# Optimization experiments

Measured on AMD Instinct MI355X. Metric: run time of the kernel, lower is better.

## Reference

```python
import jax, jax.numpy as jnp
import numpy as np

S_STA = 32          # s_sta_dim
N_TS = 4            # n_timesteps
NUM_FREQ = 4        # NeRF PE octaves -> 2 + 2*2*4 = 18 PE channels
EPS_NORM = 1e-12    # torch F.normalize default eps


def pos_enc_concat(v):
    # v: (B, C, H, W) -> concat NeRF positional encoding of pixel grid on channel dim
    B, C, H, W = v.shape
    ys = jnp.linspace(-1.0, 1.0, H)
    xs = jnp.linspace(-1.0, 1.0, W)
    coords = jnp.stack(jnp.meshgrid(ys, xs, indexing='ij'), axis=0)  # (2, H, W)
    feats = [coords]
    for i in range(NUM_FREQ):
        f = (2.0 ** i) * jnp.pi * coords
        feats.append(jnp.sin(f))
        feats.append(jnp.cos(f))
    pe = jnp.concatenate(feats, axis=0).astype(v.dtype)              # (18, H, W)
    pe = jnp.broadcast_to(pe[None], (B,) + pe.shape)
    return jnp.concatenate([v, pe], axis=1)


def setup_inputs() -> dict:
    key = jax.random.key(0)
    k1, k2, k3 = jax.random.split(key, 3)
    ch = 128
    x = jax.random.normal(k1, (4, 4, 12, ch, 24, 24), dtype=jnp.float32)
    Wv = jax.random.normal(k2, (ch, ch), dtype=jnp.float32) / np.float32(np.sqrt(ch))
    bv = jax.random.normal(k3, (ch,), dtype=jnp.float32) * 0.01
    return {"x": x, "Wv": Wv, "bv": bv, "temp": 1}


def reference(x, Wv, bv, temp):
    bs, N, T, ch, h, w = x.shape
    BN, hw = bs * N, h * w
    scale = ch ** (-0.5)
    xf = x.reshape(BN, T, ch, h, w)

    # F.normalize(p=2, dim=-3): L2-normalize over channel dim
    nrm = jnp.sqrt(jnp.sum(xf * xf, axis=2, keepdims=True))
    x_att = xf / jnp.maximum(nrm, EPS_NORM)

    qs = x_att[:, 1:].reshape(BN * (T - 1), ch, hw)
    ks = x_att[:, :-1].reshape(BN * (T - 1), ch, hw)
    energy = jnp.einsum('bcn,bcm->bnm', qs, ks).reshape(BN, T - 1, hw, hw) * scale
    attn = jax.nn.softmax(energy / temp, axis=-1)       # (BN, T-1, hw, hw)

    # to_v: 1x1 conv then NeRF PE concat
    v = jnp.einsum('oc,btchw->btohw', Wv, xf) + bv[None, None, :, None, None]
    v = pos_enc_concat(v.reshape(BN * T, ch, h, w))     # (BN*T, ch+18, h, w)
    vs_pe = v.reshape(BN, T, -1, hw)                    # (BN, T, C_v, hw)

    Tp = T - N_TS + 1
    acc = vs_pe[:, :Tp, S_STA:]                         # (BN, Tp, C_v-S_STA, hw)
    for t in range(N_TS - 1):                           # small fixed recurrence depth
        cs = vs_pe[:, t + 1:t + 1 + Tp, S_STA:]
        ca = attn[:, t:t + Tp]
        prop = jnp.einsum('btcm,btnm->btcn', acc, ca)
        acc = jnp.concatenate([cs, prop], axis=2)
    return acc
```

## Files before the change

kernel.cpp:

```cpp
#include <hip/hip_runtime.h>
#include <math.h>

#define BN 16
#define T 12
#define CH 128
#define HW 576
#define TM1 11
#define TP 9
#define CCS 114

typedef __attribute__((ext_vector_type(8))) short bf16x8;
typedef __attribute__((ext_vector_type(4))) float floatx4;

__device__ inline float b2f(unsigned short u) {
    unsigned int v = ((unsigned int)u) << 16;
    return __builtin_bit_cast(float, v);
}
__device__ inline unsigned short f2b(float f) {
    unsigned int v = __builtin_bit_cast(unsigned int, f);
    unsigned int r = (v + 0x7FFFu + ((v >> 16) & 1u)) >> 16;
    return (unsigned short)r;
}

__device__ __forceinline__ void async_copy16(void* lds, const void* g) {
    __builtin_amdgcn_global_load_lds(
        (const __attribute__((address_space(1))) unsigned int*)g,
        (__attribute__((address_space(3))) unsigned int*)lds,
        16, 0, 0);
}

__global__ __launch_bounds__(256) void k_norm_t(const float* __restrict__ x,
                                                unsigned short* __restrict__ xT) {
    int bt = blockIdx.x / 9;
    int p0 = (blockIdx.x % 9) * 64;
    int t = threadIdx.x;
    int lane = t & 63, wave = t >> 6;
    int pq = t & 15;
    int cg = t >> 4;
    const float* src = x + (size_t)bt * CH * HW + (size_t)(cg * 8) * HW + p0 + pq * 4;

    floatx4 v[8];
    float s0 = 0.f, s1 = 0.f, s2 = 0.f, s3 = 0.f;
#pragma unroll
    for (int j = 0; j < 8; j++) {
        v[j] = *(const floatx4*)(src + (size_t)j * HW);
        s0 = fmaf(v[j][0], v[j][0], s0);
        s1 = fmaf(v[j][1], v[j][1], s1);
        s2 = fmaf(v[j][2], v[j][2], s2);
        s3 = fmaf(v[j][3], v[j][3], s3);
    }
#pragma unroll
    for (int m = 16; m < 64; m <<= 1) {
        s0 += __shfl_xor(s0, m);
        s1 += __shfl_xor(s1, m);
        s2 += __shfl_xor(s2, m);
        s3 += __shfl_xor(s3, m);
    }
    __shared__ float smP[4][16][4];
    __shared__ float smI[64];
    if (lane < 16) {
        smP[wave][lane][0] = s0; smP[wave][lane][1] = s1;
        smP[wave][lane][2] = s2; smP[wave][lane][3] = s3;
    }
    __syncthreads();
    if (t < 64) {
        int q = t >> 2, k = t & 3;
        float tot = smP[0][q][k] + smP[1][q][k] + smP[2][q][k] + smP[3][q][k];
        smI[t] = 1.0f / fmaxf(sqrtf(tot), 1e-12f);
    }
    __syncthreads();
    unsigned short* dst = xT + ((size_t)bt * HW + p0 + pq * 4) * CH + cg * 8;
#pragma unroll
    for (int k = 0; k < 4; k++) {
        float inv = smI[pq * 4 + k];
        union { unsigned short u[8]; uint4 q4; } pk;
#pragma unroll
        for (int j = 0; j < 8; j++) pk.u[j] = f2b(v[j][k] * inv);
        *(uint4*)(dst + (size_t)k * CH) = pk.q4;
    }
}

__global__ __launch_bounds__(256, 2) void k_energysm(const unsigned short* __restrict__ xT,
                                                     unsigned short* __restrict__ attn,
                                                     const int* __restrict__ temp) {
    int nwg = gridDim.x;
    int wg = (blockIdx.x & 7) * (nwg >> 3) + (blockIdx.x >> 3);
    int z = wg / 18, nt = wg % 18;
    int b = z / TM1, ti = z % TM1;
    const unsigned short* Q = xT + (size_t)(b * T + ti + 1) * HW * CH;
    const unsigned short* K = xT + (size_t)(b * T + ti) * HW * CH;
    unsigned short* A = attn + (size_t)z * HW * HW;
    int n0 = nt * 32;

    int lane = threadIdx.x & 63, wave = threadIdx.x >> 6;
    int fr = lane & 15, hi = lane >> 4;
    int koff = hi * 8;
    int m0 = wave * 144;

    bf16x8 af[4][2];
#pragma unroll
    for (int k0 = 0; k0 < 4; k0++)
#pragma unroll
        for (int fi = 0; fi < 2; fi++)
            af[k0][fi] = *(const bf16x8*)(Q + (size_t)(n0 + fi * 16 + fr) * CH + k0 * 32 + koff);

    floatx4 acc[2][9] = {};
#pragma unroll
    for (int k0 = 0; k0 < 4; k0++) {
        bf16x8 bfr[9];
#pragma unroll
        for (int j = 0; j < 9; j++)
            bfr[j] = *(const bf16x8*)(K + (size_t)(m0 + j * 16 + fr) * CH + k0 * 32 + koff);
#pragma unroll
        for (int fi = 0; fi < 2; fi++)
#pragma unroll
            for (int j = 0; j < 9; j++)
                acc[fi][j] = __builtin_amdgcn_mfma_f32_16x16x32_bf16(af[k0][fi], bfr[j], acc[fi][j], 0, 0, 0);
    }

    __shared__ float smMax[4][32];
    __shared__ float smSum[4][32];
    float sc = 0.08838834764831845f / (float)temp[0];

    float pm[2][4];
#pragma unroll
    for (int fi = 0; fi < 2; fi++)
#pragma unroll
        for (int reg = 0; reg < 4; reg++) {
            float m = acc[fi][0][reg];
#pragma unroll
            for (int j = 1; j < 9; j++) m = fmaxf(m, acc[fi][j][reg]);
#pragma unroll
            for (int msk = 1; msk < 16; msk <<= 1) m = fmaxf(m, __shfl_xor(m, msk));
            pm[fi][reg] = m;
        }
    if (fr == 0) {
#pragma unroll
        for (int fi = 0; fi < 2; fi++)
#pragma unroll
            for (int reg = 0; reg < 4; reg++)
                smMax[wave][fi * 16 + hi * 4 + reg] = pm[fi][reg];
    }
    __syncthreads();

    float rmax[2][4];
#pragma unroll
    for (int fi = 0; fi < 2; fi++)
#pragma unroll
        for (int reg = 0; reg < 4; reg++) {
            int row = fi * 16 + hi * 4 + reg;
            rmax[fi][reg] = fmaxf(fmaxf(smMax[0][row], smMax[1][row]),
                                  fmaxf(smMax[2][row], smMax[3][row]));
        }

    float ps[2][4];
#pragma unroll
    for (int fi = 0; fi < 2; fi++)
#pragma unroll
        for (int reg = 0; reg < 4; reg++) {
            float s = 0.f;
#pragma unroll
            for (int j = 0; j < 9; j++) {
                float e = __expf(sc * (acc[fi][j][reg] - rmax[fi][reg]));
                acc[fi][j][reg] = e;
                s += e;
            }
#pragma unroll
            for (int msk = 1; msk < 16; msk <<= 1) s += __shfl_xor(s, msk);
            ps[fi][reg] = s;
        }
    if (fr == 0) {
#pragma unroll
        for (int fi = 0; fi < 2; fi++)
#pragma unroll
            for (int reg = 0; reg < 4; reg++)
                smSum[wave][fi * 16 + hi * 4 + reg] = ps[fi][reg];
    }
    __syncthreads();

#pragma unroll
    for (int fi = 0; fi < 2; fi++)
#pragma unroll
        for (int reg = 0; reg < 4; reg++) {
            int row = fi * 16 + hi * 4 + reg;
            float inv = 1.0f / (smSum[0][row] + smSum[1][row] + smSum[2][row] + smSum[3][row]);
            int n = n0 + row;
#pragma unroll
            for (int j = 0; j < 9; j++)
                A[(size_t)n * HW + m0 + j * 16 + fr] = f2b(acc[fi][j][reg] * inv);
        }
}

__global__ __launch_bounds__(256) void k_vgemm(const float* __restrict__ x,
                                               const float* __restrict__ Wv,
                                               const float* __restrict__ bv,
                                               unsigned short* __restrict__ cs16,
                                               float* __restrict__ out) {
    int bt = blockIdx.z;
    int b = bt / T, t = bt % T;
    const float* X = x + (size_t)bt * CH * HW;
    unsigned short* C16 = cs16 + (size_t)bt * CCS * HW;
    float* O = (t >= 3) ? out + (size_t)(b * TP + t - 3) * 456 * HW : nullptr;
    int m0 = blockIdx.y * 64, n0 = blockIdx.x * 64;
    __shared__ float As[16][66];
    __shared__ float Bs[16][66];
    int tid = threadIdx.x;
    int kq = tid % 16, lr = tid / 16;
    int tx = tid % 16, ty = tid / 16;
    int lp = tid % 64, lc = tid / 64;
    float acc[4][4] = {};
    for (int c0 = 0; c0 < CH; c0 += 16) {
#pragma unroll
        for (int i = 0; i < 4; i++) {
            int r = m0 + lr + 16 * i;
            As[kq][lr + 16 * i] = (r < 96) ? Wv[(size_t)(32 + r) * CH + c0 + kq] : 0.f;
        }
#pragma unroll
        for (int i = 0; i < 4; i++) {
            int c = lc + 4 * i;
            Bs[c][lp] = X[(size_t)(c0 + c) * HW + n0 + lp];
        }
        __syncthreads();
#pragma unroll
        for (int kk = 0; kk < 16; kk++) {
            float2 a01 = *(const float2*)&As[kk][ty * 4];
            float2 a23 = *(const float2*)&As[kk][ty * 4 + 2];
            float2 b01 = *(const float2*)&Bs[kk][tx * 4];
            float2 b23 = *(const float2*)&Bs[kk][tx * 4 + 2];
            float av[4] = {a01.x, a01.y, a23.x, a23.y};
            float bw[4] = {b01.x, b01.y, b23.x, b23.y};
#pragma unroll
            for (int i = 0; i < 4; i++)
#pragma unroll
                for (int j = 0; j < 4; j++)
                    acc[i][j] = fmaf(av[i], bw[j], acc[i][j]);
        }
        __syncthreads();
    }
#pragma unroll
    for (int i = 0; i < 4; i++) {
        int r = m0 + ty * 4 + i;
        if (r < 96) {
            float bb = bv[32 + r];
            floatx4 o;
            o[0] = acc[i][0] + bb; o[1] = acc[i][1] + bb;
            o[2] = acc[i][2] + bb; o[3] = acc[i][3] + bb;
            union { unsigned short u[4]; uint2 v; } pk;
            pk.u[0] = f2b(o[0]); pk.u[1] = f2b(o[1]); pk.u[2] = f2b(o[2]); pk.u[3] = f2b(o[3]);
            *(uint2*)(C16 + (size_t)r * HW + n0 + tx * 4) = pk.v;
            if (O) __builtin_nontemporal_store(o, (floatx4*)(O + (size_t)r * HW + n0 + tx * 4));
        }
    }
}

__global__ __launch_bounds__(576) void k_pe(unsigned short* __restrict__ cs16,
                                            float* __restrict__ out) {
    int bt = blockIdx.x;
    int b = bt / T, t = bt % T;
    int p = threadIdx.x;
    unsigned short* C16 = cs16 + ((size_t)bt * CCS + 96) * HW + p;
    float* O = (t >= 3) ? out + ((size_t)(b * TP + t - 3) * 456 + 96) * HW + p : nullptr;
    int iy = p / 24, ix = p % 24;
    float y = -1.f + 2.f * (float)iy / 23.f;
    float xx = -1.f + 2.f * (float)ix / 23.f;
    float vals[18];
    vals[0] = y; vals[1] = xx;
    const float PI = 3.14159265358979323846f;
#pragma unroll
    for (int i = 0; i < 4; i++) {
        float k = (float)(1 << i) * PI;
        float fy = k * y, fx = k * xx;
        vals[2 + 4 * i + 0] = sinf(fy);
        vals[2 + 4 * i + 1] = sinf(fx);
        vals[2 + 4 * i + 2] = cosf(fy);
        vals[2 + 4 * i + 3] = cosf(fx);
    }
#pragma unroll
    for (int c = 0; c < 18; c++) {
        C16[(size_t)c * HW] = f2b(vals[c]);
        if (O) __builtin_nontemporal_store(vals[c], O + (size_t)c * HW);
    }
}

template<int M_, bool F32OUT>
__global__ __launch_bounds__(256) void k_stage(const unsigned short* __restrict__ cs16,
                                               const unsigned short* __restrict__ prop_in,
                                               const unsigned short* __restrict__ attn,
                                               float* __restrict__ dst_f32,
                                               unsigned short* __restrict__ dst_b16,
                                               int tshift, int prop_ch,
                                               int dst_stride_ch, int dst_ch_off) {
    constexpr int MT = (M_ + 127) / 128;
    constexpr int WPZ = MT * 6;
    constexpr int BUFSZ = 28672;

    int nwg = gridDim.x;
    int wg = (blockIdx.x & 7) * (nwg >> 3) + (blockIdx.x >> 3);
    int z = wg / WPZ;
    int rem = wg % WPZ;
    int mt = rem / 6, nt = rem % 6;
    int m0 = mt * 128, n0 = nt * 96;

    int b = z / TP, tp = z % TP;
    const unsigned short* csz = cs16 + (size_t)((b * T + tp + tshift) * CCS) * HW;
    const unsigned short* prz = prop_in ? prop_in + (size_t)z * prop_ch * HW : csz;
    const unsigned short* Bm = attn + (size_t)(b * TM1 + tp + tshift) * HW * HW;

    __shared__ uint4 smq[2 * BUFSZ / 16];
    char* smc = (char*)smq;

    int tid = threadIdx.x;
    int lane = tid & 63, wave = tid >> 6;
    int wm = wave >> 1, wn = wave & 1;
    int fr = lane & 15, hi = lane >> 4;

    int cp = tid & 7;
    int rloc = tid >> 3;
    const unsigned short* srcA[4];
#pragma unroll
    for (int i = 0; i < 4; i++) {
        int r = i * 32 + rloc;
        int rg = m0 + r;
        const unsigned short* p;
        if (rg < CCS) p = csz + (size_t)rg * HW;
        else if (rg < M_) p = prz + (size_t)(rg - CCS) * HW;
        else p = csz;
        srcA[i] = p + ((cp ^ (r & 7)) << 3);
    }
    const unsigned short* srcB[3];
#pragma unroll
    for (int i = 0; i < 3; i++) {
        int r = i * 32 + rloc;
        srcB[i] = Bm + (size_t)(n0 + r) * HW + ((cp ^ (r & 7)) << 3);
    }

    int arow[4], brow[3];
#pragma unroll
    for (int i = 0; i < 4; i++) arow[i] = (wm * 64 + i * 16 + fr) * 128;
#pragma unroll
    for (int j = 0; j < 3; j++) brow[j] = (wn * 48 + j * 16 + fr) * 128;
    int xr = fr & 7;

    floatx4 acc[4][3] = {};
    int buf = 0;

    {
        char* base = smc;
        int wo = wave * 1024;
#pragma unroll
        for (int i = 0; i < 4; i++) async_copy16(base + i * 4096 + wo, srcA[i]);
#pragma unroll
        for (int i = 0; i < 3; i++) async_copy16(base + 16384 + i * 4096 + wo, srcB[i]);
    }
    __syncthreads();

    for (int t = 0; t < 9; ++t) {
        if (t < 8) {
            char* nb = smc + (buf ^ 1) * BUFSZ;
            int wo = wave * 1024;
            int ko = (t + 1) * 64;
#pragma unroll
            for (int i = 0; i < 4; i++) async_copy16(nb + i * 4096 + wo, srcA[i] + ko);
#pragma unroll
            for (int i = 0; i < 3; i++) async_copy16(nb + 16384 + i * 4096 + wo, srcB[i] + ko);
        }
        char* base = smc + buf * BUFSZ;
#pragma unroll
        for (int s = 0; s < 2; ++s) {
            int coff = ((s * 4 + hi) ^ xr) << 4;
            bf16x8 af[4], bfr[3];
#pragma unroll
            for (int i = 0; i < 4; i++) af[i] = *(const bf16x8*)(base + arow[i] + coff);
#pragma unroll
            for (int j = 0; j < 3; j++) bfr[j] = *(const bf16x8*)(base + 16384 + brow[j] + coff);
#pragma unroll
            for (int i = 0; i < 4; i++)
#pragma unroll
                for (int j = 0; j < 3; j++)
                    acc[i][j] = __builtin_amdgcn_mfma_f32_16x16x32_bf16(af[i], bfr[j], acc[i][j], 0, 0, 0);
        }
        __syncthreads();
        buf ^= 1;
    }

    int crow = hi * 4, ccol = fr;
#pragma unroll
    for (int i = 0; i < 4; i++) {
#pragma unroll
        for (int reg = 0; reg < 4; reg++) {
            int r = m0 + wm * 64 + i * 16 + crow + reg;
            if (r < M_) {
#pragma unroll
                for (int j = 0; j < 3; j++) {
                    int n = n0 + wn * 48 + j * 16 + ccol;
                    size_t idx = ((size_t)z * dst_stride_ch + dst_ch_off + r) * HW + n;
                    if (F32OUT) __builtin_nontemporal_store(acc[i][j][reg], dst_f32 + idx);
                    else dst_b16[idx] = f2b(acc[i][j][reg]);
                }
            }
        }
    }
}

extern "C" void kernel_launch(void* const* d_in, const int* in_sizes, int n_in,
                              void* d_out, int out_size, void* d_ws, size_t ws_size,
                              hipStream_t stream) {
    const float* x  = (const float*)d_in[0];
    const float* Wv = (const float*)d_in[1];
    const float* bv = (const float*)d_in[2];
    const int* temp = (const int*)d_in[3];
    float* out = (float*)d_out;

    char* w = (char*)d_ws;
    unsigned short* xT     = (unsigned short*)w;
    w += (size_t)192 * HW * CH * 2;
    unsigned short* attn16 = (unsigned short*)w;
    w += (size_t)176 * HW * HW * 2;
    unsigned short* cs16   = (unsigned short*)w;
    w += (size_t)192 * CCS * HW * 2;
    unsigned short* p1     = (unsigned short*)w;
    w += (size_t)144 * CCS * HW * 2;
    unsigned short* p2     = (unsigned short*)w;

    k_norm_t<<<192 * 9, 256, 0, stream>>>(x, xT);
    k_energysm<<<dim3(3168), 256, 0, stream>>>(xT, attn16, temp);
    k_vgemm<<<dim3(9, 2, 192), 256, 0, stream>>>(x, Wv, bv, cs16, out);
    k_pe<<<192, 576, 0, stream>>>(cs16, out);
    k_stage<114, false><<<dim3(864),  256, 0, stream>>>(cs16, nullptr, attn16, nullptr, p1, 0, 0, 114, 0);
    k_stage<228, false><<<dim3(1728), 256, 0, stream>>>(cs16, p1, attn16, nullptr, p2, 1, 114, 228, 0);
    k_stage<342, true ><<<dim3(2592), 256, 0, stream>>>(cs16, p2, attn16, out, nullptr, 2, 228, 456, 114);
}
```

Baseline: 486.0 us.

## Stage K tiles through double-buffered swizzled LDS with async copies in energy-softmax kernel

The energy/softmax kernel used to load K fragments straight from global memory into registers for every k-step. Each block now copies K into LDS with async 16-byte copies, double-buffered over the 4 k-steps, using an XOR swizzle to avoid bank conflicts, and the MFMAs read from LDS. This shares K loads across the block and overlaps the next slice's copy with the current MFMAs. In exchange it uses about 72KB of LDS per block, which may limit occupancy below the launch_bounds target of 2 blocks, and adds a barrier per step.

```diff
diff --git a/kernel.cpp b/kernel.cpp
--- a/kernel.cpp
+++ b/kernel.cpp
@@ -94,32 +94,59 @@
 
     int lane = threadIdx.x & 63, wave = threadIdx.x >> 6;
     int fr = lane & 15, hi = lane >> 4;
-    int koff = hi * 8;
     int m0 = wave * 144;
 
-    bf16x8 af[4][2];
-#pragma unroll
-    for (int k0 = 0; k0 < 4; k0++)
-#pragma unroll
-        for (int fi = 0; fi < 2; fi++)
-            af[k0][fi] = *(const bf16x8*)(Q + (size_t)(n0 + fi * 16 + fr) * CH + k0 * 32 + koff);
-
-    floatx4 acc[2][9] = {};
-#pragma unroll
-    for (int k0 = 0; k0 < 4; k0++) {
-        bf16x8 bfr[9];
-#pragma unroll
-        for (int j = 0; j < 9; j++)
-            bfr[j] = *(const bf16x8*)(K + (size_t)(m0 + j * 16 + fr) * CH + k0 * 32 + koff);
-#pragma unroll
-        for (int fi = 0; fi < 2; fi++)
-#pragma unroll
-            for (int j = 0; j < 9; j++)
-                acc[fi][j] = __builtin_amdgcn_mfma_f32_16x16x32_bf16(af[k0][fi], bfr[j], acc[fi][j], 0, 0, 0);
-    }
-
+    __shared__ char smB[2 * 36864];
     __shared__ float smMax[4][32];
     __shared__ float smSum[4][32];
+
+    bf16x8 af[4][2];
+#pragma unroll
+    for (int k0 = 0; k0 < 4; k0++)
+#pragma unroll
+        for (int fi = 0; fi < 2; fi++)
+            af[k0][fi] = *(const bf16x8*)(Q + (size_t)(n0 + fi * 16 + fr) * CH + k0 * 32 + hi * 8);
+
+    int tt = threadIdx.x;
+    int rw = tt >> 2;
+    int scp = (tt & 3) ^ ((rw >> 1) & 3);
+    const unsigned short* srcB[9];
+#pragma unroll
+    for (int g = 0; g < 9; g++)
+        srcB[g] = K + (size_t)(g * 64 + rw) * CH + scp * 8;
+
+    int xc = (fr >> 1) & 3;
+    int boff[9];
+#pragma unroll
+    for (int j = 0; j < 9; j++)
+        boff[j] = (m0 + j * 16 + fr) * 64 + ((hi ^ xc) << 4);
+
+#pragma unroll
+    for (int g = 0; g < 9; g++)
+        async_copy16(smB + g * 4096 + wave * 1024, srcB[g]);
+    __syncthreads();
+
+    floatx4 acc[2][9] = {};
+#pragma unroll
+    for (int s = 0; s < 4; s++) {
+        if (s < 3) {
+            char* nb = smB + ((s + 1) & 1) * 36864 + wave * 1024;
+#pragma unroll
+            for (int g = 0; g < 9; g++)
+                async_copy16(nb + g * 4096, srcB[g] + (s + 1) * 32);
+        }
+        const char* cb = smB + (s & 1) * 36864;
+        bf16x8 bfr[9];
+#pragma unroll
+        for (int j = 0; j < 9; j++) bfr[j] = *(const bf16x8*)(cb + boff[j]);
+#pragma unroll
+        for (int fi = 0; fi < 2; fi++)
+#pragma unroll
+            for (int j = 0; j < 9; j++)
+                acc[fi][j] = __builtin_amdgcn_mfma_f32_16x16x32_bf16(af[s][fi], bfr[j], acc[fi][j], 0, 0, 0);
+        __syncthreads();
+    }
+
     float sc = 0.08838834764831845f / (float)temp[0];
 
     float pm[2][4];
```

After: 479.4 us. Within noise of the previous version (-1.3%).
